# Kernel tuning notes

Hardware: AMD Instinct MI355X
Metric: run time of the kernel (lower is better)

## Reference

```python
import jax, jax.numpy as jnp
import numpy as np

L = 4          # num_layers
H = 128        # hidden_channels
F = 128        # num_filters
G = 25         # num_gaussians
N = 10000      # nodes
E = 320000     # radius-graph edges
EH = 40000     # hull edges
NG = 64        # graphs in batch
CUTOFF = 5.0
PI = float(np.pi)
LOG2 = float(np.log(2.0))


def ssp(x):  # ShiftedSoftplus
    return jax.nn.softplus(x) - LOG2


def setup_inputs() -> dict:
    key = jax.random.key(0)
    ks = iter(jax.random.split(key, 64))
    w = lambda shape: jax.random.normal(next(ks), shape, jnp.float32) * 0.05
    inp = {
        'z': jax.random.randint(next(ks), (N,), 0, 100),
        'edge_index': jax.random.randint(next(ks), (2, E), 0, N),
        'edge_index_hull': jax.random.randint(next(ks), (2, EH), 0, N),
        'batch': jnp.sort(jax.random.randint(next(ks), (N,), 0, NG)),
        'dist': jax.random.uniform(next(ks), (E,), jnp.float32) * CUTOFF,
        'fea_hull': jax.random.normal(next(ks), (EH, 7), jnp.float32),
        'emb_table': w((100, H)),
        'lin_w': w((L, F, H)),
        'mlp_w1': w((L, F, G)), 'mlp_b1': jnp.zeros((L, F), jnp.float32),
        'mlp_w2': w((L, F, F)), 'mlp_b2': jnp.zeros((L, F), jnp.float32),
        'linh_w': w((L, F, H)),
        'mlph_w1': w((L, F, 7)), 'mlph_b1': jnp.zeros((L, F), jnp.float32),
        'mlph_w2': w((L, F, F)), 'mlph_b2': jnp.zeros((L, F), jnp.float32),
        'v1_w': w((L, H, F)), 'v1_b': jnp.zeros((L, H), jnp.float32),
        'v2_w': w((L, 64, H)), 'v2_b': jnp.zeros((L, 64), jnp.float32),
        'vh1_w': w((L, H, F)), 'vh1_b': jnp.zeros((L, H), jnp.float32),
        'vh2_w': w((L, 64, H)), 'vh2_b': jnp.zeros((L, 64), jnp.float32),
        'cat_w': w((L, H, 128)), 'cat_b': jnp.zeros((L, H), jnp.float32),
        'u1_w': w((64, H)), 'u1_b': jnp.zeros((64,), jnp.float32),
        'u2_w': w((1, 64)), 'u2_b': jnp.zeros((1,), jnp.float32),
    }
    return inp


def reference(z, edge_index, edge_index_hull, batch, dist, fea_hull, emb_table,
              lin_w, mlp_w1, mlp_b1, mlp_w2, mlp_b2,
              linh_w, mlph_w1, mlph_b1, mlph_w2, mlph_b2,
              v1_w, v1_b, v2_w, v2_b, vh1_w, vh1_b, vh2_w, vh2_b,
              cat_w, cat_b, u1_w, u1_b, u2_w, u2_b):
    n = z.shape[0]
    # Gaussian distance embedding: emb(0, cutoff, G)
    offset = jnp.linspace(0.0, CUTOFF, G)
    coeff = -0.5 / (offset[1] - offset[0]) ** 2
    dist_emb = jnp.exp(coeff * (dist[:, None] - offset[None, :]) ** 2)  # [E,G]
    C = 0.5 * (jnp.cos(dist * PI / CUTOFF) + 1.0)                       # [E]
    j, i = edge_index[0], edge_index[1]
    jh, ih = edge_index_hull[0], edge_index_hull[1]
    v = emb_table[z]                                                    # [N,H]
    for l in range(L):
        # update_e
        W = (ssp(dist_emb @ mlp_w1[l].T + mlp_b1[l]) @ mlp_w2[l].T + mlp_b2[l]) * C[:, None]
        e = (v @ lin_w[l].T)[j] * W                                     # [E,F]
        Wh = ssp(fea_hull @ mlph_w1[l].T + mlph_b1[l]) @ mlph_w2[l].T + mlph_b2[l]
        eh = (v @ linh_w[l].T)[jh] * Wh                                 # [EH,F]
        # update_v
        out = jax.ops.segment_sum(e, i, num_segments=n)
        out = ssp(out @ v1_w[l].T + v1_b[l]) @ v2_w[l].T + v2_b[l]      # [N,64]
        outh = jax.ops.segment_sum(eh, ih, num_segments=n)
        outh = ssp(outh @ vh1_w[l].T + vh1_b[l]) @ vh2_w[l].T + vh2_b[l]
        v = v + ssp(jnp.concatenate([out, outh], axis=1) @ cat_w[l].T + cat_b[l])
    # update_u
    u = ssp(v @ u1_w.T + u1_b) @ u2_w.T + u2_b                          # [N,1]
    return jax.ops.segment_sum(u, batch, num_segments=NG)               # [NG,1]
```

## Files before the change

kernel.cpp:

```cpp
#include <hip/hip_runtime.h>
#include <hip/hip_bf16.h>

typedef __hip_bfloat16 bf16;
typedef unsigned short ushort;
typedef __attribute__((ext_vector_type(8))) short short8;
typedef __attribute__((ext_vector_type(4))) float f32x4;

__device__ __forceinline__ float dssp(float x){
  return fmaxf(x, 0.f) + __logf(1.f + __expf(-fabsf(x))) - 0.693147180559945f;
}
__device__ __forceinline__ int clampi(int x, int lo, int hi){ return x<lo?lo:(x>hi?hi:x); }
__device__ __forceinline__ ushort f2b(float f){
  unsigned x = __float_as_uint(f);
  return (ushort)((x + 0x7fffu + ((x>>16)&1u)) >> 16);
}
__device__ __forceinline__ float b2f16(ushort u){ return __uint_as_float(((unsigned)u)<<16); }

constexpr int TBL_K    = 4096;
constexpr int TBL_ROWS = TBL_K + 1;
constexpr int TBL_TILES = (TBL_ROWS + 31) / 32;

__global__ void detect_mode(const unsigned* __restrict__ raw, int* flag){
  __shared__ int c;
  int t = threadIdx.x;
  if (t==0) c = 0;
  __syncthreads();
  unsigned u  = raw[t];
  unsigned lo = u & 0xFFFFu;
  int e = (int)((lo >> 7) & 0xFF);
  int ok = (lo==0u) || (e >= 0x70 && e <= 0x8F);
  atomicAdd(&c, ok);
  __syncthreads();
  if (t==0) *flag = (c >= 160) ? 1 : 0;
}

struct Seg { const void* src; float* dst; int n; };
struct SegTable { Seg s[27]; int count; long total; };

__global__ void convert_all(SegTable tbl, const int* __restrict__ flag){
  int mode = *flag;
  long tid    = (long)blockIdx.x*blockDim.x + threadIdx.x;
  long stride = (long)gridDim.x*blockDim.x;
  for (long i=tid; i<tbl.total; i+=stride){
    long off = i; int k = 0;
    while (k < tbl.count-1 && off >= tbl.s[k].n){ off -= tbl.s[k].n; k++; }
    float f;
    if (mode) f = __bfloat162float(((const bf16*)tbl.s[k].src)[off]);
    else      f = ((const float*)tbl.s[k].src)[off];
    tbl.s[k].dst[off] = (f==f) ? f : 0.f;
  }
}

struct WSeg { const float* src; ushort* dst; int n; };
struct WTable { WSeg s[9]; int count; int total; };

__global__ void convert_wb(WTable wt){
  int tid = blockIdx.x*blockDim.x + threadIdx.x;
  if (tid >= wt.total) return;
  int off = tid, k = 0;
  while (k < wt.count-1 && off >= wt.s[k].n){ off -= wt.s[k].n; k++; }
  wt.s[k].dst[off] = f2b(wt.s[k].src[off]);
}

__global__ void init_all(int* cnt_r, int* cnt_h, float* uacc,
                         int2* spk_r, int2* spk_h, int N, int E, int EH){
  int t = blockIdx.x*blockDim.x + threadIdx.x;
  if (t < N){ cnt_r[t]=0; cnt_h[t]=0; }
  if (t < 64) uacc[t]=0.f;
  if (t < E)  spk_r[t]=make_int2(0,0);
  if (t < EH) spk_h[t]=make_int2(0,0);
}

__global__ void count_edges(const int* __restrict__ ei, const int* __restrict__ eih,
                            int E, int EH, int N, int* cnt_r, int* cnt_h){
  int t = blockIdx.x*blockDim.x + threadIdx.x;
  if (t < E)  atomicAdd(&cnt_r[clampi(ei[E + t], 0, N-1)], 1);
  if (t < EH) atomicAdd(&cnt_h[clampi(eih[EH + t], 0, N-1)], 1);
}

__global__ __launch_bounds__(1024) void scan_pair(const int* cnt_r, int* off_r, int* cur_r,
                                                  const int* cnt_h, int* off_h, int* cur_h, int N){
  __shared__ int s[1024];
  int t = threadIdx.x;
  int CH = (N + 1023) / 1024;
  for (int which=0; which<2; which++){
    const int* cnt = which? cnt_h : cnt_r;
    int* off = which? off_h : off_r;
    int* cur = which? cur_h : cur_r;
    int base = t*CH;
    int sum = 0;
    for (int q=0;q<CH;q++){ int idx=base+q; sum += (idx<N)? cnt[idx] : 0; }
    __syncthreads();
    s[t]=sum; __syncthreads();
    for (int ofs=1; ofs<1024; ofs<<=1){
      int v = s[t]; int vp = (t>=ofs)? s[t-ofs] : 0;
      __syncthreads(); s[t]=v+vp; __syncthreads();
    }
    int run = (t>0)? s[t-1] : 0;
    for (int q=0;q<CH;q++){
      int idx=base+q;
      if (idx<N){ off[idx]=run; cur[idx]=run; run += cnt[idx]; }
    }
    if (t==1023) off[N] = s[1023];
  }
}

__global__ void scatter_edges(const int* __restrict__ ei, const float* __restrict__ distc,
                              const int* __restrict__ eih, int E, int EH, int N,
                              int* cur_r, int* cur_h, int2* spk_r, int2* spk_h){
  int t = blockIdx.x*blockDim.x + threadIdx.x;
  if (t < E){
    int i = clampi(ei[E+t], 0, N-1);
    int p = clampi(atomicAdd(&cur_r[i], 1), 0, E-1);
    float x = fminf(fmaxf(distc[t]*(4096.0f/5.0f), 0.f), 4095.999f);
    int i0 = (int)x; if (i0 > TBL_K-1) i0 = TBL_K-1;
    unsigned fr16 = (unsigned)((x - (float)i0)*65536.0f); if (fr16 > 65535u) fr16 = 65535u;
    spk_r[p] = make_int2(clampi(ei[t],0,N-1), (int)(((unsigned)i0<<16)|fr16));
  }
  if (t < EH){
    int ih = clampi(eih[EH+t], 0, N-1);
    int p = clampi(atomicAdd(&cur_h[ih], 1), 0, EH-1);
    spk_h[p] = make_int2(clampi(eih[t],0,N-1), t);
  }
}

__global__ __launch_bounds__(256) void build_wtab(const float* __restrict__ mlp_w1,
    const float* __restrict__ mlp_b1, const float* __restrict__ mlp_w2,
    const float* __restrict__ mlp_b2, ushort* __restrict__ Wtab){
  int l    = blockIdx.x / TBL_TILES;
  int tile = blockIdx.x % TBL_TILES;
  int row0 = tile * 32;
  const float* w1 = mlp_w1 + l*128*25;
  const float* b1 = mlp_b1 + l*128;
  const float* w2 = mlp_w2 + l*128*128;
  const float* b2 = mlp_b2 + l*128;
  __shared__ float Gs[32][26];
  __shared__ float Ts[32][129];
  __shared__ float Ws[32][129];
  int t = threadIdx.x;
  for (int idx=t; idx<32*25; idx+=256){
    int r = idx/25, k = idx%25;
    float d = (row0+r) * (5.0f/4096.0f);
    float x = d - (float)k*(5.0f/24.0f);
    Gs[r][k] = __expf(-11.52f*x*x);
  }
  __syncthreads();
  int rg = t&7, cg = t>>3;
  #pragma unroll
  for (int ri=0;ri<4;ri++){
    int r = rg*4+ri;
    #pragma unroll
    for (int ci=0;ci<4;ci++){
      int c = cg*4+ci;
      float s = b1[c];
      for (int k=0;k<25;k++) s += Gs[r][k]*w1[c*25+k];
      Ts[r][c] = dssp(s);
    }
  }
  float acc[4][4] = {};
  for (int k0=0;k0<128;k0+=32){
    __syncthreads();
    for (int idx=t; idx<1024; idx+=256){
      int c=idx>>3, kk4=(idx&7)*4;
      float4 f = *(const float4*)(w2+(size_t)c*128+k0+kk4);
      Ws[kk4][c]=f.x; Ws[kk4+1][c]=f.y; Ws[kk4+2][c]=f.z; Ws[kk4+3][c]=f.w;
    }
    __syncthreads();
    for (int kk=0;kk<32;kk++){
      float xv[4];
      #pragma unroll
      for (int ri=0;ri<4;ri++) xv[ri]=Ts[rg*4+ri][k0+kk];
      #pragma unroll
      for (int ci=0;ci<4;ci++){
        float wv = Ws[kk][cg*4+ci];
        #pragma unroll
        for (int ri=0;ri<4;ri++) acc[ri][ci] += xv[ri]*wv;
      }
    }
  }
  #pragma unroll
  for (int ri=0;ri<4;ri++){
    int r = row0 + rg*4 + ri;
    if (r >= TBL_ROWS) continue;
    float d  = r * (5.0f/4096.0f);
    float Cf = 0.5f*(cosf(d*(3.14159265358979f/5.0f))+1.0f);
    #pragma unroll
    for (int ci=0;ci<4;ci++){
      int c = cg*4+ci;
      Wtab[((size_t)l*TBL_ROWS + r)*128 + c] = f2b((acc[ri][ci] + b2[c]) * Cf);
    }
  }
}

__global__ void pack_wtab(const ushort* __restrict__ Wtab, unsigned* __restrict__ Wpk){
  long t = (long)blockIdx.x*blockDim.x + threadIdx.x;
  const long TOT = 4L*TBL_K*128;
  if (t < TOT){
    int l = (int)(t / ((long)TBL_K*128));
    long rem = t % ((long)TBL_K*128);
    int r = (int)(rem >> 7), f = (int)(rem & 127);
    const ushort* base = Wtab + (size_t)l*TBL_ROWS*128;
    Wpk[t] = (((unsigned)base[(size_t)(r+1)*128+f])<<16) | (unsigned)base[(size_t)r*128+f];
  }
}

__device__ __forceinline__ short8 afragb(const ushort (*Xb)[136], int lane, int k0){
  int m=lane&15, q=(lane>>4)&3;
  return *(const short8*)(&Xb[m][k0+q*8]);
}
__device__ __forceinline__ short8 bfrag(const ushort* __restrict__ W, int cbase, int lane, int k0){
  int n=lane&15, q=(lane>>4)&3;
  return *(const short8*)(W + (size_t)(cbase+n)*128 + k0 + q*8);
}
template<int NT>
__device__ __forceinline__ void mgemm(const ushort (*Xb)[136],
    const ushort* __restrict__ W, int t, f32x4 d[NT]){
  int lane=t&63, w=t>>6;
  #pragma unroll
  for (int ct=0;ct<NT;ct++) d[ct]=(f32x4){0.f,0.f,0.f,0.f};
  #pragma unroll
  for (int kc=0;kc<4;kc++){
    short8 a = afragb(Xb, lane, kc*32);
    #pragma unroll
    for (int ct=0;ct<NT;ct++){
      short8 b = bfrag(W, w*(NT*16)+ct*16, lane, kc*32);
      d[ct] = __builtin_amdgcn_mfma_f32_16x16x32_bf16(a, b, d[ct], 0, 0, 0);
    }
  }
}
template<int NT>
__device__ __forceinline__ void d2tile(ushort (*Y)[136], const f32x4 d[NT], int t,
    int colofs, const float* __restrict__ bias, int do_ssp){
  int lane=t&63, w=t>>6, q=(lane>>4)&3, n=lane&15;
  #pragma unroll
  for (int ct=0;ct<NT;ct++){
    int c = w*(NT*16)+ct*16+n;
    float bv = bias? bias[c] : 0.f;
    #pragma unroll
    for (int i=0;i<4;i++){
      float y = d[ct][i] + bv;
      if (do_ssp) y = dssp(y);
      Y[q*4+i][colofs+c] = f2b(y);
    }
  }
}
template<int NT>
__device__ __forceinline__ void d2os(float (*Os)[132], const f32x4 d[NT], int t,
    const float* __restrict__ bias, int do_ssp){
  int lane=t&63, w=t>>6, q=(lane>>4)&3, n=lane&15;
  #pragma unroll
  for (int ct=0;ct<NT;ct++){
    int c = w*(NT*16)+ct*16+n;
    float bv = bias? bias[c] : 0.f;
    #pragma unroll
    for (int i=0;i<4;i++){
      float y = d[ct][i] + bv;
      if (do_ssp) y = dssp(y);
      Os[q*4+i][c] = y;
    }
  }
}
__device__ __forceinline__ void d2glob_c(ushort* __restrict__ out, const f32x4 d[2],
    int t, int row0, int N, ushort (*Tmp)[136]){
  d2tile<2>(Tmp, d, t, 0, nullptr, 0);
  __syncthreads();
  int r=t>>4, o=(t&15)*8;
  int gr=row0+r;
  if (gr<N) *(uint4*)(out + (size_t)gr*128 + o) = *(const uint4*)&Tmp[r][o];
  __syncthreads();
}

__global__ __launch_bounds__(256) void f_first(const int* __restrict__ z,
    const float* __restrict__ emb, float* __restrict__ v,
    const ushort* __restrict__ linA, const ushort* __restrict__ linB,
    ushort* __restrict__ vlin, ushort* __restrict__ vlinh, int N){
  __shared__ ushort Xb[16][136];
  __shared__ ushort Tb[16][136];
  int t=threadIdx.x; int row0=blockIdx.x*16;
  f32x4 d[2];
  for (int idx=t; idx<512; idx+=256){
    int r=idx>>5, k4=(idx&31)*4; int gr=row0+r;
    int zz=(gr<N)? clampi(z[gr],0,99):0;
    float4 f = *(const float4*)(emb + (size_t)zz*128 + k4);
    unsigned r0 = (unsigned)f2b(f.x) | ((unsigned)f2b(f.y)<<16);
    unsigned r1 = (unsigned)f2b(f.z) | ((unsigned)f2b(f.w)<<16);
    *(uint2*)&Xb[r][k4] = make_uint2(r0,r1);
    if (gr<N) *(float4*)(v + (size_t)gr*128 + k4) = f;
  }
  __syncthreads();
  mgemm<2>(Xb, linA, t, d);
  d2glob_c(vlin, d, t, row0, N, Tb);
  mgemm<2>(Xb, linB, t, d);
  d2glob_c(vlinh, d, t, row0, N, Tb);
}

__global__ __launch_bounds__(256) void f_mid(
    const float* __restrict__ accR, const float* __restrict__ accH,
    float* __restrict__ v,
    const ushort* __restrict__ v1w, const float* __restrict__ v1b,
    const ushort* __restrict__ v2w, const float* __restrict__ v2b,
    const ushort* __restrict__ vh1w, const float* __restrict__ vh1b,
    const ushort* __restrict__ vh2w, const float* __restrict__ vh2b,
    const ushort* __restrict__ cw, const float* __restrict__ cb,
    const ushort* __restrict__ linA, const ushort* __restrict__ linB,
    ushort* __restrict__ vlin, ushort* __restrict__ vlinh, int N){
  __shared__ ushort Xb[16][136];
  __shared__ ushort Xb2[16][136];
  __shared__ ushort Xb3[16][136];
  __shared__ float  Os[16][132];
  int t=threadIdx.x; int row0=blockIdx.x*16;
  f32x4 d[2]; f32x4 d1[1];

  for (int path=0; path<2; path++){
    const float* X = path? accH : accR;
    __syncthreads();
    for (int idx=t; idx<512; idx+=256){
      int r=idx>>5, k4=(idx&31)*4; int gr=row0+r;
      float4 f=(gr<N)? *(const float4*)(X+(size_t)gr*128+k4):make_float4(0,0,0,0);
      unsigned r0 = (unsigned)f2b(f.x) | ((unsigned)f2b(f.y)<<16);
      unsigned r1 = (unsigned)f2b(f.z) | ((unsigned)f2b(f.w)<<16);
      *(uint2*)&Xb[r][k4] = make_uint2(r0,r1);
    }
    __syncthreads();
    mgemm<2>(Xb, path?vh1w:v1w, t, d);
    d2tile<2>(Xb2, d, t, 0, path?vh1b:v1b, 1);
    __syncthreads();
    mgemm<1>(Xb2, path?vh2w:v2w, t, d1);
    d2tile<1>(Xb3, d1, t, path*64, path?vh2b:v2b, 0);
  }
  __syncthreads();
  mgemm<2>(Xb3, cw, t, d);
  d2os<2>(Os, d, t, cb, 1);
  __syncthreads();
  for (int idx=t; idx<512; idx+=256){
    int r=idx>>5, k4=(idx&31)*4; int gr=row0+r;
    float4 f=(gr<N)? *(const float4*)(v+(size_t)gr*128+k4):make_float4(0,0,0,0);
    f.x+=Os[r][k4]; f.y+=Os[r][k4+1]; f.z+=Os[r][k4+2]; f.w+=Os[r][k4+3];
    if (gr<N) *(float4*)(v+(size_t)gr*128+k4)=f;
    unsigned r0 = (unsigned)f2b(f.x) | ((unsigned)f2b(f.y)<<16);
    unsigned r1 = (unsigned)f2b(f.z) | ((unsigned)f2b(f.w)<<16);
    *(uint2*)&Xb[r][k4] = make_uint2(r0,r1);
  }
  __syncthreads();
  mgemm<2>(Xb, linA, t, d);
  d2glob_c(vlin, d, t, row0, N, Xb2);
  mgemm<2>(Xb, linB, t, d);
  d2glob_c(vlinh, d, t, row0, N, Xb2);
}

__global__ __launch_bounds__(256) void f_last(
    const float* __restrict__ accR, const float* __restrict__ accH,
    const float* __restrict__ v,
    const ushort* __restrict__ v1w, const float* __restrict__ v1b,
    const ushort* __restrict__ v2w, const float* __restrict__ v2b,
    const ushort* __restrict__ vh1w, const float* __restrict__ vh1b,
    const ushort* __restrict__ vh2w, const float* __restrict__ vh2b,
    const ushort* __restrict__ cw, const float* __restrict__ cb,
    const ushort* __restrict__ u1w, const float* __restrict__ u1b,
    const float* __restrict__ u2w, const float* __restrict__ u2b,
    const int* __restrict__ batch, float* __restrict__ uacc, int N){
  __shared__ ushort Xb[16][136];
  __shared__ ushort Xb2[16][136];
  __shared__ ushort Xb3[16][136];
  __shared__ float  Os[16][132];
  __shared__ float ss[16];
  __shared__ int   bb[16];
  int t=threadIdx.x; int row0=blockIdx.x*16;
  f32x4 d[2]; f32x4 d1[1];

  for (int path=0; path<2; path++){
    const float* X = path? accH : accR;
    __syncthreads();
    for (int idx=t; idx<512; idx+=256){
      int r=idx>>5, k4=(idx&31)*4; int gr=row0+r;
      float4 f=(gr<N)? *(const float4*)(X+(size_t)gr*128+k4):make_float4(0,0,0,0);
      unsigned r0 = (unsigned)f2b(f.x) | ((unsigned)f2b(f.y)<<16);
      unsigned r1 = (unsigned)f2b(f.z) | ((unsigned)f2b(f.w)<<16);
      *(uint2*)&Xb[r][k4] = make_uint2(r0,r1);
    }
    __syncthreads();
    mgemm<2>(Xb, path?vh1w:v1w, t, d);
    d2tile<2>(Xb2, d, t, 0, path?vh1b:v1b, 1);
    __syncthreads();
    mgemm<1>(Xb2, path?vh2w:v2w, t, d1);
    d2tile<1>(Xb3, d1, t, path*64, path?vh2b:v2b, 0);
  }
  __syncthreads();
  mgemm<2>(Xb3, cw, t, d);
  d2os<2>(Os, d, t, cb, 1);
  __syncthreads();
  for (int idx=t; idx<512; idx+=256){
    int r=idx>>5, k4=(idx&31)*4; int gr=row0+r;
    float4 f=(gr<N)? *(const float4*)(v+(size_t)gr*128+k4):make_float4(0,0,0,0);
    f.x+=Os[r][k4]; f.y+=Os[r][k4+1]; f.z+=Os[r][k4+2]; f.w+=Os[r][k4+3];
    unsigned r0 = (unsigned)f2b(f.x) | ((unsigned)f2b(f.y)<<16);
    unsigned r1 = (unsigned)f2b(f.z) | ((unsigned)f2b(f.w)<<16);
    *(uint2*)&Xb[r][k4] = make_uint2(r0,r1);
  }
  __syncthreads();
  mgemm<1>(Xb, u1w, t, d1);
  d2os<1>(Os, d1, t, u1b, 1);
  __syncthreads();
  if (t<16){
    int gr=row0+t;
    float s=0.f; int bt=-1;
    if (gr<N){
      s = u2b[0];
      for (int c=0;c<64;c++) s += Os[t][c]*u2w[c];
      bt = clampi(batch[gr],0,63);
    }
    ss[t]=s; bb[t]=bt;
  }
  __syncthreads();
  if (t==0){
    float run=0.f; int cur=-1;
    for (int q=0;q<16;q++){
      int bq=bb[q];
      if (bq<0) continue;
      if (bq!=cur){ if (cur>=0) atomicAdd(&uacc[cur],run); cur=bq; run=0.f; }
      run += ss[q];
    }
    if (cur>=0) atomicAdd(&uacc[cur],run);
  }
}

__global__ __launch_bounds__(256) void hull_all(const int2* __restrict__ spk_h,
    const float* __restrict__ fea,
    const float* __restrict__ mlph_w1, const float* __restrict__ mlph_b1,
    const ushort* __restrict__ mlph_w2b, const float* __restrict__ mlph_b2,
    ushort* __restrict__ WhS_base, size_t lstride,
    int EH, int tilesPerLayer, int l0){
  int l    = l0 + blockIdx.x / tilesPerLayer;
  int tile = blockIdx.x % tilesPerLayer;
  int row0 = tile*64;
  const float* w1 = mlph_w1 + l*128*7;
  const float* b1 = mlph_b1 + l*128;
  const ushort* w2 = mlph_w2b + (size_t)l*16384;
  const float* b2 = mlph_b2 + l*128;
  ushort* WhS = WhS_base + (size_t)(l-l0)*lstride;
  __shared__ int   Eid[64];
  __shared__ float Fs[64][8];
  __shared__ ushort Buf[64][136];
  int t=threadIdx.x;
  if (t < 64){
    int p=row0+t;
    Eid[t]=(p<EH)? clampi(spk_h[p].y,0,EH-1):0;
  }
  __syncthreads();
  for (int idx=t; idx<448; idx+=256){
    int r=idx/7, k=idx%7;
    int p=row0+r;
    Fs[r][k]=(p<EH)? fea[(size_t)Eid[r]*7+k]:0.f;
  }
  __syncthreads();
  {
    int c0=(t&31)*4, r0=(t>>5)*8;
    float w[4][7]; float bb[4];
    #pragma unroll
    for (int cc=0;cc<4;cc++){
      bb[cc]=b1[c0+cc];
      #pragma unroll
      for (int k=0;k<7;k++) w[cc][k]=w1[(c0+cc)*7+k];
    }
    #pragma unroll
    for (int rr=0;rr<8;rr++){
      int r=r0+rr;
      float fv[7];
      #pragma unroll
      for (int k=0;k<7;k++) fv[k]=Fs[r][k];
      ushort o[4];
      #pragma unroll
      for (int cc=0;cc<4;cc++){
        float s=bb[cc];
        #pragma unroll
        for (int k=0;k<7;k++) s=fmaf(fv[k],w[cc][k],s);
        o[cc]=f2b(dssp(s));
      }
      unsigned lo=(unsigned)o[0]|((unsigned)o[1]<<16);
      unsigned hi=(unsigned)o[2]|((unsigned)o[3]<<16);
      *(uint2*)&Buf[r][c0]=make_uint2(lo,hi);
    }
  }
  __syncthreads();
  int lane=t&63, w=t>>6;
  const ushort (*Xw)[136] = (const ushort (*)[136])&Buf[w*16][0];
  f32x4 d[8];
  #pragma unroll
  for (int ct=0;ct<8;ct++) d[ct]=(f32x4){0.f,0.f,0.f,0.f};
  #pragma unroll
  for (int kc=0;kc<4;kc++){
    short8 a = afragb(Xw, lane, kc*32);
    #pragma unroll
    for (int ct=0;ct<8;ct++){
      short8 b = bfrag(w2, ct*16, lane, kc*32);
      d[ct] = __builtin_amdgcn_mfma_f32_16x16x32_bf16(a, b, d[ct], 0, 0, 0);
    }
  }
  __syncthreads();
  int q=(lane>>4)&3, n=lane&15;
  #pragma unroll
  for (int ct=0;ct<8;ct++){
    int c=ct*16+n;
    float bv=b2[c];
    #pragma unroll
    for (int i=0;i<4;i++)
      Buf[w*16+q*4+i][c] = f2b(d[ct][i]+bv);
  }
  __syncthreads();
  #pragma unroll
  for (int j=0;j<4;j++){
    int idx=j*256+t;
    int r=idx>>4, o=(idx&15)*8;
    *(uint4*)(WhS + (size_t)(row0+r)*128 + o) = *(const uint4*)&Buf[r][o];
  }
}

__device__ __forceinline__ float rlerp(unsigned y, const unsigned* __restrict__ Wpk, int f){
  int i0 = (int)(y>>16);
  float fr = (float)(y&0xFFFFu)*(1.f/65536.f);
  unsigned u = Wpk[(size_t)i0*128+f];
  float w0=__uint_as_float(u<<16), w1=__uint_as_float(u&0xFFFF0000u);
  return fmaf(fr, w1-w0, w0);
}

__global__ __launch_bounds__(128) void acc_both(
    const int* __restrict__ off_r, const int2* __restrict__ spk_r,
    const ushort* __restrict__ vlin, const unsigned* __restrict__ Wpk,
    float* __restrict__ accR,
    const int* __restrict__ off_h, const int2* __restrict__ spk_h,
    const ushort* __restrict__ vlinh, const ushort* __restrict__ WhS,
    float* __restrict__ accH,
    int Etot, int EHtot, int N){
  int f = threadIdx.x;
  if ((int)blockIdx.x < N){
    int n = blockIdx.x;
    int b = clampi(off_r[n], 0, Etot);
    int e = clampi(off_r[n+1], b, Etot);
    float a = 0.f;
    int p = b;
    for (; p+8<=e; p+=8){
      int2 k[8];
      #pragma unroll
      for (int j=0;j<8;j++) k[j]=spk_r[p+j];
      float vv[8], ww[8];
      #pragma unroll
      for (int j=0;j<8;j++) vv[j]=b2f16(vlin[(size_t)k[j].x*128+f]);
      #pragma unroll
      for (int j=0;j<8;j++) ww[j]=rlerp((unsigned)k[j].y, Wpk, f);
      #pragma unroll
      for (int j=0;j<8;j++) a=fmaf(vv[j],ww[j],a);
    }
    for (; p+4<=e; p+=4){
      int2 k0=spk_r[p], k1=spk_r[p+1], k2=spk_r[p+2], k3=spk_r[p+3];
      float v0 = b2f16(vlin[(size_t)k0.x*128+f]);
      float v1 = b2f16(vlin[(size_t)k1.x*128+f]);
      float v2 = b2f16(vlin[(size_t)k2.x*128+f]);
      float v3 = b2f16(vlin[(size_t)k3.x*128+f]);
      float w0 = rlerp((unsigned)k0.y, Wpk, f);
      float w1 = rlerp((unsigned)k1.y, Wpk, f);
      float w2 = rlerp((unsigned)k2.y, Wpk, f);
      float w3 = rlerp((unsigned)k3.y, Wpk, f);
      a += v0*w0 + v1*w1 + v2*w2 + v3*w3;
    }
    for (; p<e; p++){
      int2 k0=spk_r[p];
      a += b2f16(vlin[(size_t)k0.x*128+f]) * rlerp((unsigned)k0.y, Wpk, f);
    }
    accR[(size_t)n*128+f] = a;
  } else {
    int n = blockIdx.x - N;
    int b = clampi(off_h[n], 0, EHtot);
    int e = clampi(off_h[n+1], b, EHtot);
    float a = 0.f;
    int p = b;
    for (; p+4<=e; p+=4){
      int2 k0=spk_h[p], k1=spk_h[p+1], k2=spk_h[p+2], k3=spk_h[p+3];
      float v0 = b2f16(vlinh[(size_t)k0.x*128+f]);
      float v1 = b2f16(vlinh[(size_t)k1.x*128+f]);
      float v2 = b2f16(vlinh[(size_t)k2.x*128+f]);
      float v3 = b2f16(vlinh[(size_t)k3.x*128+f]);
      a += v0*b2f16(WhS[(size_t)p*128+f])     + v1*b2f16(WhS[(size_t)(p+1)*128+f])
         + v2*b2f16(WhS[(size_t)(p+2)*128+f]) + v3*b2f16(WhS[(size_t)(p+3)*128+f]);
    }
    for (; p<e; p++){
      int2 k0=spk_h[p];
      a += b2f16(vlinh[(size_t)k0.x*128+f]) * b2f16(WhS[(size_t)p*128+f]);
    }
    accH[(size_t)n*128+f] = a;
  }
}

__global__ void write_out(const float* __restrict__ uacc, void* out, const int* __restrict__ flag){
  int t = threadIdx.x;
  if (t < 64){
    if (*flag) ((bf16*)out)[t] = __float2bfloat16(uacc[t]);
    else       ((float*)out)[t] = uacc[t];
  }
}

extern "C" void kernel_launch(void* const* d_in, const int* in_sizes, int n_in,
                              void* d_out, int out_size, void* d_ws, size_t ws_size,
                              hipStream_t stream){
  const int* z     = (const int*)d_in[0];
  const int* ei    = (const int*)d_in[1];
  const int* eih   = (const int*)d_in[2];
  const int* batch = (const int*)d_in[3];

  const int N  = in_sizes[0];
  const int E  = in_sizes[1]/2;
  const int EH = in_sizes[2]/2;
  const int EHpad = (EH + 63) & ~63;

  char* wp = (char*)d_ws;
  auto alloc = [&](size_t bytes)->char*{
    char* p = wp; wp += (bytes + 255) & ~(size_t)255; return p;
  };
  int* flag    = (int*)alloc(256);
  int* cnt_r   = (int*)alloc((size_t)N*4);
  int* off_r   = (int*)alloc((size_t)(N+1)*4);
  int* cur_r   = (int*)alloc((size_t)N*4);
  int* cnt_h   = (int*)alloc((size_t)N*4);
  int* off_h   = (int*)alloc((size_t)(N+1)*4);
  int* cur_h   = (int*)alloc((size_t)N*4);
  int2* spk_r  = (int2*)alloc((size_t)E*8);
  int2* spk_h  = (int2*)alloc((size_t)EH*8);
  float* uacc  = (float*)alloc(64*4);

  SegTable tbl; tbl.count = 27; tbl.total = 0;
  float* cvt[27];
  for (int i=0;i<27;i++){
    int n = in_sizes[4+i];
    cvt[i] = (float*)alloc((size_t)n*4);
    tbl.s[i].src = d_in[4+i];
    tbl.s[i].dst = cvt[i];
    tbl.s[i].n   = n;
    tbl.total   += n;
  }
  const float* distc   = cvt[0];
  const float* feac    = cvt[1];
  const float* embc    = cvt[2];
  const float* mlp_w1  = cvt[4];
  const float* mlp_b1  = cvt[5];
  const float* mlp_w2  = cvt[6];
  const float* mlp_b2  = cvt[7];
  const float* mlph_w1 = cvt[9];
  const float* mlph_b1 = cvt[10];
  const float* mlph_b2 = cvt[12];
  const float* v1_b  = cvt[14];
  const float* v2_b  = cvt[16];
  const float* vh1_b = cvt[18];
  const float* vh2_b = cvt[20];
  const float* cat_b = cvt[22];
  const float* u1_b  = cvt[24];
  const float* u2_w  = cvt[25];
  const float* u2_b  = cvt[26];

  ushort* lin_wb   = (ushort*)alloc((size_t)4*16384*2);
  ushort* linh_wb  = (ushort*)alloc((size_t)4*16384*2);
  ushort* v1_wb    = (ushort*)alloc((size_t)4*16384*2);
  ushort* vh1_wb   = (ushort*)alloc((size_t)4*16384*2);
  ushort* cat_wb   = (ushort*)alloc((size_t)4*16384*2);
  ushort* mlph_w2b = (ushort*)alloc((size_t)4*16384*2);
  ushort* v2_wb    = (ushort*)alloc((size_t)4*8192*2);
  ushort* vh2_wb   = (ushort*)alloc((size_t)4*8192*2);
  ushort* u1_wb    = (ushort*)alloc((size_t)8192*2);
  WTable wt; wt.count = 9;
  wt.s[0] = { cvt[3],  lin_wb,   4*16384 };
  wt.s[1] = { cvt[8],  linh_wb,  4*16384 };
  wt.s[2] = { cvt[13], v1_wb,    4*16384 };
  wt.s[3] = { cvt[17], vh1_wb,   4*16384 };
  wt.s[4] = { cvt[21], cat_wb,   4*16384 };
  wt.s[5] = { cvt[11], mlph_w2b, 4*16384 };
  wt.s[6] = { cvt[15], v2_wb,    4*8192  };
  wt.s[7] = { cvt[19], vh2_wb,   4*8192  };
  wt.s[8] = { cvt[23], u1_wb,    8192    };
  wt.total = 6*4*16384 + 2*4*8192 + 8192;

  ushort*   Wtab = (ushort*)alloc((size_t)4*TBL_ROWS*128*2);
  unsigned* Wpk  = (unsigned*)alloc((size_t)4*TBL_K*128*4);
  float* v     = (float*)alloc((size_t)N*128*4);
  ushort* vlin  = (ushort*)alloc((size_t)N*128*2);
  ushort* vlinh = (ushort*)alloc((size_t)N*128*2);
  float* accR  = (float*)alloc((size_t)N*128*4);
  float* accH  = (float*)alloc((size_t)N*128*4);

  size_t used = (size_t)(wp - (char*)d_ws);
  size_t whs1 = (size_t)EHpad*128*2;
  bool pre = (ws_size >= used + 4*whs1 + 256);
  ushort* WhS = (ushort*)alloc(pre ? 4*whs1 : whs1);

  detect_mode<<<1,256,0,stream>>>((const unsigned*)d_in[6], flag);
  {
    int cb = (int)((tbl.total + 255)/256);
    if (cb > 4096) cb = 4096;
    convert_all<<<cb,256,0,stream>>>(tbl, flag);
  }
  convert_wb<<<(wt.total+255)/256,256,0,stream>>>(wt);

  int nb;
  nb = (E+255)/256;     init_all<<<nb,256,0,stream>>>(cnt_r,cnt_h,uacc,spk_r,spk_h,N,E,EH);
  nb = (E+255)/256;     count_edges<<<nb,256,0,stream>>>(ei,eih,E,EH,N,cnt_r,cnt_h);
  scan_pair<<<1,1024,0,stream>>>(cnt_r,off_r,cur_r,cnt_h,off_h,cur_h,N);
  nb = (E+255)/256;     scatter_edges<<<nb,256,0,stream>>>(ei,distc,eih,E,EH,N,cur_r,cur_h,spk_r,spk_h);
  build_wtab<<<4*TBL_TILES,256,0,stream>>>(mlp_w1,mlp_b1,mlp_w2,mlp_b2,Wtab);
  pack_wtab<<<(int)((4L*TBL_K*128+255)/256),256,0,stream>>>(Wtab,Wpk);

  const int nt = (N+15)/16;
  const int ht64 = (EH+63)/64;
  if (pre)
    hull_all<<<4*ht64,256,0,stream>>>(spk_h, feac, mlph_w1, mlph_b1, mlph_w2b, mlph_b2,
                                      WhS, whs1/2, EH, ht64, 0);

  f_first<<<nt,256,0,stream>>>(z, embc, v, lin_wb, linh_wb, vlin, vlinh, N);
  for (int l=0;l<4;l++){
    if (!pre)
      hull_all<<<ht64,256,0,stream>>>(spk_h, feac, mlph_w1, mlph_b1, mlph_w2b, mlph_b2,
                                      WhS, 0, EH, ht64, l);
    const ushort* WhSl = pre ? (WhS + (size_t)l*(whs1/2)) : WhS;
    acc_both<<<2*N,128,0,stream>>>(off_r, spk_r, vlin, Wpk + (size_t)l*TBL_K*128, accR,
                                   off_h, spk_h, vlinh, WhSl, accH, E, EH, N);
    if (l<3){
      f_mid<<<nt,256,0,stream>>>(accR, accH, v,
          v1_wb + (size_t)l*16384, v1_b + l*128, v2_wb + (size_t)l*8192, v2_b + l*64,
          vh1_wb + (size_t)l*16384, vh1_b + l*128, vh2_wb + (size_t)l*8192, vh2_b + l*64,
          cat_wb + (size_t)l*16384, cat_b + l*128,
          lin_wb + (size_t)(l+1)*16384, linh_wb + (size_t)(l+1)*16384, vlin, vlinh, N);
    } else {
      f_last<<<nt,256,0,stream>>>(accR, accH, v,
          v1_wb + (size_t)l*16384, v1_b + l*128, v2_wb + (size_t)l*8192, v2_b + l*64,
          vh1_wb + (size_t)l*16384, vh1_b + l*128, vh2_wb + (size_t)l*8192, vh2_b + l*64,
          cat_wb + (size_t)l*16384, cat_b + l*128,
          u1_wb, u1_b, u2_w, u2_b, batch, uacc, N);
    }
  }
  write_out<<<1,64,0,stream>>>(uacc, d_out, flag);
}
```

Measured before the change: 485.5 us.

## Merge setup kernels into fewer launches and convert weights directly from inputs

```diff
diff --git a/kernel.cpp b/kernel.cpp
--- a/kernel.cpp
+++ b/kernel.cpp
@@ -20,62 +20,68 @@
 constexpr int TBL_ROWS = TBL_K + 1;
 constexpr int TBL_TILES = (TBL_ROWS + 31) / 32;
 
-__global__ void detect_mode(const unsigned* __restrict__ raw, int* flag){
+struct Seg { const void* src; float* dst; int n; };
+struct SegTable { Seg s[18]; int count; long total; };
+struct WSeg { const void* src; ushort* dst; int n; };
+struct WTable { WSeg s[9]; int count; int total; };
+
+__global__ void setup_all(const unsigned* __restrict__ raw, int* flag,
+                          int* cnt_r, int* cnt_h, float* uacc,
+                          int2* spk_r, int2* spk_h, int N, int E, int EH){
   __shared__ int c;
-  int t = threadIdx.x;
-  if (t==0) c = 0;
-  __syncthreads();
-  unsigned u  = raw[t];
-  unsigned lo = u & 0xFFFFu;
-  int e = (int)((lo >> 7) & 0xFF);
-  int ok = (lo==0u) || (e >= 0x70 && e <= 0x8F);
-  atomicAdd(&c, ok);
-  __syncthreads();
-  if (t==0) *flag = (c >= 160) ? 1 : 0;
-}
-
-struct Seg { const void* src; float* dst; int n; };
-struct SegTable { Seg s[27]; int count; long total; };
-
-__global__ void convert_all(SegTable tbl, const int* __restrict__ flag){
-  int mode = *flag;
-  long tid    = (long)blockIdx.x*blockDim.x + threadIdx.x;
-  long stride = (long)gridDim.x*blockDim.x;
-  for (long i=tid; i<tbl.total; i+=stride){
-    long off = i; int k = 0;
-    while (k < tbl.count-1 && off >= tbl.s[k].n){ off -= tbl.s[k].n; k++; }
-    float f;
-    if (mode) f = __bfloat162float(((const bf16*)tbl.s[k].src)[off]);
-    else      f = ((const float*)tbl.s[k].src)[off];
-    tbl.s[k].dst[off] = (f==f) ? f : 0.f;
-  }
-}
-
-struct WSeg { const float* src; ushort* dst; int n; };
-struct WTable { WSeg s[9]; int count; int total; };
-
-__global__ void convert_wb(WTable wt){
-  int tid = blockIdx.x*blockDim.x + threadIdx.x;
-  if (tid >= wt.total) return;
-  int off = tid, k = 0;
-  while (k < wt.count-1 && off >= wt.s[k].n){ off -= wt.s[k].n; k++; }
-  wt.s[k].dst[off] = f2b(wt.s[k].src[off]);
-}
-
-__global__ void init_all(int* cnt_r, int* cnt_h, float* uacc,
-                         int2* spk_r, int2* spk_h, int N, int E, int EH){
   int t = blockIdx.x*blockDim.x + threadIdx.x;
   if (t < N){ cnt_r[t]=0; cnt_h[t]=0; }
   if (t < 64) uacc[t]=0.f;
   if (t < E)  spk_r[t]=make_int2(0,0);
   if (t < EH) spk_h[t]=make_int2(0,0);
-}
-
-__global__ void count_edges(const int* __restrict__ ei, const int* __restrict__ eih,
-                            int E, int EH, int N, int* cnt_r, int* cnt_h){
-  int t = blockIdx.x*blockDim.x + threadIdx.x;
-  if (t < E)  atomicAdd(&cnt_r[clampi(ei[E + t], 0, N-1)], 1);
-  if (t < EH) atomicAdd(&cnt_h[clampi(eih[EH + t], 0, N-1)], 1);
+  if (blockIdx.x==0){
+    if (threadIdx.x==0) c=0;
+    __syncthreads();
+    unsigned u  = raw[threadIdx.x];
+    unsigned lo = u & 0xFFFFu;
+    int e = (int)((lo >> 7) & 0xFF);
+    int ok = (lo==0u) || (e >= 0x70 && e <= 0x8F);
+    atomicAdd(&c, ok);
+    __syncthreads();
+    if (threadIdx.x==0) *flag = (c >= 160) ? 1 : 0;
+  }
+}
+
+__global__ __launch_bounds__(256) void convert_count(SegTable tbl, WTable wt,
+    const int* __restrict__ flag,
+    const int* __restrict__ ei, const int* __restrict__ eih,
+    int E, int EH, int N, int* cnt_r, int* cnt_h, int CA, int CB){
+  int b = blockIdx.x;
+  if (b < CA){
+    int mode = *flag;
+    long tid    = (long)b*256 + threadIdx.x;
+    long stride = (long)CA*256;
+    for (long i=tid; i<tbl.total; i+=stride){
+      long off = i; int k = 0;
+      while (k < tbl.count-1 && off >= tbl.s[k].n){ off -= tbl.s[k].n; k++; }
+      float f;
+      if (mode) f = __bfloat162float(((const bf16*)tbl.s[k].src)[off]);
+      else      f = ((const float*)tbl.s[k].src)[off];
+      tbl.s[k].dst[off] = (f==f) ? f : 0.f;
+    }
+  } else if (b < CA+CB){
+    int mode = *flag;
+    long tid    = (long)(b-CA)*256 + threadIdx.x;
+    long stride = (long)CB*256;
+    for (long i=tid; i<wt.total; i+=stride){
+      long off = i; int k = 0;
+      while (k < wt.count-1 && off >= wt.s[k].n){ off -= wt.s[k].n; k++; }
+      if (mode) wt.s[k].dst[off] = ((const ushort*)wt.s[k].src)[off];
+      else {
+        float f = ((const float*)wt.s[k].src)[off];
+        wt.s[k].dst[off] = f2b((f==f)? f : 0.f);
+      }
+    }
+  } else {
+    int t = (b-CA-CB)*256 + threadIdx.x;
+    if (t < E)  atomicAdd(&cnt_r[clampi(ei[E + t], 0, N-1)], 1);
+    if (t < EH) atomicAdd(&cnt_h[clampi(eih[EH + t], 0, N-1)], 1);
+  }
 }
 
 __global__ __launch_bounds__(1024) void scan_pair(const int* cnt_r, int* off_r, int* cur_r,
@@ -105,38 +111,42 @@
   }
 }
 
-__global__ void scatter_edges(const int* __restrict__ ei, const float* __restrict__ distc,
-                              const int* __restrict__ eih, int E, int EH, int N,
-                              int* cur_r, int* cur_h, int2* spk_r, int2* spk_h){
-  int t = blockIdx.x*blockDim.x + threadIdx.x;
-  if (t < E){
-    int i = clampi(ei[E+t], 0, N-1);
-    int p = clampi(atomicAdd(&cur_r[i], 1), 0, E-1);
-    float x = fminf(fmaxf(distc[t]*(4096.0f/5.0f), 0.f), 4095.999f);
-    int i0 = (int)x; if (i0 > TBL_K-1) i0 = TBL_K-1;
-    unsigned fr16 = (unsigned)((x - (float)i0)*65536.0f); if (fr16 > 65535u) fr16 = 65535u;
-    spk_r[p] = make_int2(clampi(ei[t],0,N-1), (int)(((unsigned)i0<<16)|fr16));
-  }
-  if (t < EH){
-    int ih = clampi(eih[EH+t], 0, N-1);
-    int p = clampi(atomicAdd(&cur_h[ih], 1), 0, EH-1);
-    spk_h[p] = make_int2(clampi(eih[t],0,N-1), t);
-  }
-}
-
-__global__ __launch_bounds__(256) void build_wtab(const float* __restrict__ mlp_w1,
-    const float* __restrict__ mlp_b1, const float* __restrict__ mlp_w2,
-    const float* __restrict__ mlp_b2, ushort* __restrict__ Wtab){
-  int l    = blockIdx.x / TBL_TILES;
-  int tile = blockIdx.x % TBL_TILES;
+__global__ __launch_bounds__(256) void scatter_build(
+    const int* __restrict__ ei, const float* __restrict__ distc,
+    const int* __restrict__ eih, int E, int EH, int N,
+    int* cur_r, int* cur_h, int2* spk_r, int2* spk_h,
+    const float* __restrict__ mlp_w1, const float* __restrict__ mlp_b1,
+    const float* __restrict__ mlp_w2, const float* __restrict__ mlp_b2,
+    ushort* __restrict__ Wtab, int nbE){
+  __shared__ __align__(16) char smem[36352];
+  if ((int)blockIdx.x < nbE){
+    int t = blockIdx.x*256 + threadIdx.x;
+    if (t < E){
+      int i = clampi(ei[E+t], 0, N-1);
+      int p = clampi(atomicAdd(&cur_r[i], 1), 0, E-1);
+      float x = fminf(fmaxf(distc[t]*(4096.0f/5.0f), 0.f), 4095.999f);
+      int i0 = (int)x; if (i0 > TBL_K-1) i0 = TBL_K-1;
+      unsigned fr16 = (unsigned)((x - (float)i0)*65536.0f); if (fr16 > 65535u) fr16 = 65535u;
+      spk_r[p] = make_int2(clampi(ei[t],0,N-1), (int)(((unsigned)i0<<16)|fr16));
+    }
+    if (t < EH){
+      int ih = clampi(eih[EH+t], 0, N-1);
+      int p = clampi(atomicAdd(&cur_h[ih], 1), 0, EH-1);
+      spk_h[p] = make_int2(clampi(eih[t],0,N-1), t);
+    }
+    return;
+  }
+  int bid  = blockIdx.x - nbE;
+  int l    = bid / TBL_TILES;
+  int tile = bid % TBL_TILES;
   int row0 = tile * 32;
   const float* w1 = mlp_w1 + l*128*25;
   const float* b1 = mlp_b1 + l*128;
   const float* w2 = mlp_w2 + l*128*128;
   const float* b2 = mlp_b2 + l*128;
-  __shared__ float Gs[32][26];
-  __shared__ float Ts[32][129];
-  __shared__ float Ws[32][129];
+  float (*Gs)[26]  = (float(*)[26])smem;
+  float (*Ts)[129] = (float(*)[129])(smem+3328);
+  float (*Ws)[129] = (float(*)[129])(smem+19840);
   int t = threadIdx.x;
   for (int idx=t; idx<32*25; idx+=256){
     int r = idx/25, k = idx%25;
@@ -192,18 +202,6 @@
   }
 }
 
-__global__ void pack_wtab(const ushort* __restrict__ Wtab, unsigned* __restrict__ Wpk){
-  long t = (long)blockIdx.x*blockDim.x + threadIdx.x;
-  const long TOT = 4L*TBL_K*128;
-  if (t < TOT){
-    int l = (int)(t / ((long)TBL_K*128));
-    long rem = t % ((long)TBL_K*128);
-    int r = (int)(rem >> 7), f = (int)(rem & 127);
-    const ushort* base = Wtab + (size_t)l*TBL_ROWS*128;
-    Wpk[t] = (((unsigned)base[(size_t)(r+1)*128+f])<<16) | (unsigned)base[(size_t)r*128+f];
-  }
-}
-
 __device__ __forceinline__ short8 afragb(const ushort (*Xb)[136], int lane, int k0){
   int m=lane&15, q=(lane>>4)&3;
   return *(const short8*)(&Xb[m][k0+q*8]);
@@ -270,13 +268,104 @@
   __syncthreads();
 }
 
-__global__ __launch_bounds__(256) void f_first(const int* __restrict__ z,
+__device__ void hull_body(int bid, const int2* __restrict__ spk_h,
+    const float* __restrict__ fea,
+    const float* __restrict__ mlph_w1, const float* __restrict__ mlph_b1,
+    const ushort* __restrict__ mlph_w2b, const float* __restrict__ mlph_b2,
+    ushort* __restrict__ WhS_base, size_t lstride,
+    int EH, int tilesPerLayer, int l0, char* smem){
+  int l    = l0 + bid / tilesPerLayer;
+  int tile = bid % tilesPerLayer;
+  int row0 = tile*64;
+  const float* w1 = mlph_w1 + l*128*7;
+  const float* b1 = mlph_b1 + l*128;
+  const ushort* w2 = mlph_w2b + (size_t)l*16384;
+  const float* b2 = mlph_b2 + l*128;
+  ushort* WhS = WhS_base + (size_t)(l-l0)*lstride;
+  int*   Eid = (int*)smem;
+  float (*Fs)[8] = (float(*)[8])(smem+256);
+  ushort (*Buf)[136] = (ushort(*)[136])(smem+2304);
+  int t=threadIdx.x;
+  if (t < 64){
+    int p=row0+t;
+    Eid[t]=(p<EH)? clampi(spk_h[p].y,0,EH-1):0;
+  }
+  __syncthreads();
+  for (int idx=t; idx<448; idx+=256){
+    int r=idx/7, k=idx%7;
+    int p=row0+r;
+    Fs[r][k]=(p<EH)? fea[(size_t)Eid[r]*7+k]:0.f;
+  }
+  __syncthreads();
+  {
+    int c0=(t&31)*4, r0=(t>>5)*8;
+    float w[4][7]; float bb[4];
+    #pragma unroll
+    for (int cc=0;cc<4;cc++){
+      bb[cc]=b1[c0+cc];
+      #pragma unroll
+      for (int k=0;k<7;k++) w[cc][k]=w1[(c0+cc)*7+k];
+    }
+    #pragma unroll
+    for (int rr=0;rr<8;rr++){
+      int r=r0+rr;
+      float fv[7];
+      #pragma unroll
+      for (int k=0;k<7;k++) fv[k]=Fs[r][k];
+      ushort o[4];
+      #pragma unroll
+      for (int cc=0;cc<4;cc++){
+        float s=bb[cc];
+        #pragma unroll
+        for (int k=0;k<7;k++) s=fmaf(fv[k],w[cc][k],s);
+        o[cc]=f2b(dssp(s));
+      }
+      unsigned lo=(unsigned)o[0]|((unsigned)o[1]<<16);
+      unsigned hi=(unsigned)o[2]|((unsigned)o[3]<<16);
+      *(uint2*)&Buf[r][c0]=make_uint2(lo,hi);
+    }
+  }
+  __syncthreads();
+  int lane=t&63, w=t>>6;
+  const ushort (*Xw)[136] = (const ushort (*)[136])&Buf[w*16][0];
+  f32x4 d[8];
+  #pragma unroll
+  for (int ct=0;ct<8;ct++) d[ct]=(f32x4){0.f,0.f,0.f,0.f};
+  #pragma unroll
+  for (int kc=0;kc<4;kc++){
+    short8 a = afragb(Xw, lane, kc*32);
+    #pragma unroll
+    for (int ct=0;ct<8;ct++){
+      short8 b = bfrag(w2, ct*16, lane, kc*32);
+      d[ct] = __builtin_amdgcn_mfma_f32_16x16x32_bf16(a, b, d[ct], 0, 0, 0);
+    }
+  }
+  __syncthreads();
+  int q=(lane>>4)&3, n=lane&15;
+  #pragma unroll
+  for (int ct=0;ct<8;ct++){
+    int c=ct*16+n;
+    float bv=b2[c];
+    #pragma unroll
+    for (int i=0;i<4;i++)
+      Buf[w*16+q*4+i][c] = f2b(d[ct][i]+bv);
+  }
+  __syncthreads();
+  #pragma unroll
+  for (int j=0;j<4;j++){
+    int idx=j*256+t;
+    int r=idx>>4, o=(idx&15)*8;
+    *(uint4*)(WhS + (size_t)(row0+r)*128 + o) = *(const uint4*)&Buf[r][o];
+  }
+}
+
+__device__ void f_first_body(int bid, const int* __restrict__ z,
     const float* __restrict__ emb, float* __restrict__ v,
     const ushort* __restrict__ linA, const ushort* __restrict__ linB,
-    ushort* __restrict__ vlin, ushort* __restrict__ vlinh, int N){
-  __shared__ ushort Xb[16][136];
-  __shared__ ushort Tb[16][136];
-  int t=threadIdx.x; int row0=blockIdx.x*16;
+    ushort* __restrict__ vlin, ushort* __restrict__ vlinh, int N, char* smem){
+  ushort (*Xb)[136] = (ushort(*)[136])smem;
+  ushort (*Tb)[136] = (ushort(*)[136])(smem+4352);
+  int t=threadIdx.x; int row0=bid*16;
   f32x4 d[2];
   for (int idx=t; idx<512; idx+=256){
     int r=idx>>5, k4=(idx&31)*4; int gr=row0+r;
@@ -292,6 +381,47 @@
   d2glob_c(vlin, d, t, row0, N, Tb);
   mgemm<2>(Xb, linB, t, d);
   d2glob_c(vlinh, d, t, row0, N, Tb);
+}
+
+__global__ __launch_bounds__(256) void hull_pack_first(const int2* __restrict__ spk_h,
+    const float* __restrict__ fea,
+    const float* __restrict__ mlph_w1, const float* __restrict__ mlph_b1,
+    const ushort* __restrict__ mlph_w2b, const float* __restrict__ mlph_b2,
+    ushort* __restrict__ WhS, size_t lstride, int EH, int ht64,
+    const int* __restrict__ z, const float* __restrict__ emb, float* __restrict__ v,
+    const ushort* __restrict__ linA, const ushort* __restrict__ linB,
+    ushort* __restrict__ vlin, ushort* __restrict__ vlinh, int N, int nt,
+    const ushort* __restrict__ Wtab, unsigned* __restrict__ Wpk, int PB, int HB){
+  __shared__ __align__(16) char smem[19968];
+  int b = blockIdx.x;
+  if (b < HB){
+    hull_body(b, spk_h, fea, mlph_w1, mlph_b1, mlph_w2b, mlph_b2,
+              WhS, lstride, EH, ht64, 0, smem);
+  } else if (b < HB+nt){
+    f_first_body(b-HB, z, emb, v, linA, linB, vlin, vlinh, N, smem);
+  } else {
+    long tid    = (long)(b-HB-nt)*256 + threadIdx.x;
+    long stride = (long)PB*256;
+    const long TOT = 4L*TBL_K*128;
+    for (long i=tid; i<TOT; i+=stride){
+      int l = (int)(i / ((long)TBL_K*128));
+      long rem = i % ((long)TBL_K*128);
+      int r = (int)(rem >> 7), f = (int)(rem & 127);
+      const ushort* base = Wtab + (size_t)l*TBL_ROWS*128;
+      Wpk[i] = (((unsigned)base[(size_t)(r+1)*128+f])<<16) | (unsigned)base[(size_t)r*128+f];
+    }
+  }
+}
+
+__global__ __launch_bounds__(256) void hull_all(const int2* __restrict__ spk_h,
+    const float* __restrict__ fea,
+    const float* __restrict__ mlph_w1, const float* __restrict__ mlph_b1,
+    const ushort* __restrict__ mlph_w2b, const float* __restrict__ mlph_b2,
+    ushort* __restrict__ WhS_base, size_t lstride,
+    int EH, int tilesPerLayer, int l0){
+  __shared__ __align__(16) char smem[19968];
+  hull_body(blockIdx.x, spk_h, fea, mlph_w1, mlph_b1, mlph_w2b, mlph_b2,
+            WhS_base, lstride, EH, tilesPerLayer, l0, smem);
 }
 
 __global__ __launch_bounds__(256) void f_mid(
@@ -424,97 +554,6 @@
   }
 }
 
-__global__ __launch_bounds__(256) void hull_all(const int2* __restrict__ spk_h,
-    const float* __restrict__ fea,
-    const float* __restrict__ mlph_w1, const float* __restrict__ mlph_b1,
-    const ushort* __restrict__ mlph_w2b, const float* __restrict__ mlph_b2,
-    ushort* __restrict__ WhS_base, size_t lstride,
-    int EH, int tilesPerLayer, int l0){
-  int l    = l0 + blockIdx.x / tilesPerLayer;
-  int tile = blockIdx.x % tilesPerLayer;
-  int row0 = tile*64;
-  const float* w1 = mlph_w1 + l*128*7;
-  const float* b1 = mlph_b1 + l*128;
-  const ushort* w2 = mlph_w2b + (size_t)l*16384;
-  const float* b2 = mlph_b2 + l*128;
-  ushort* WhS = WhS_base + (size_t)(l-l0)*lstride;
-  __shared__ int   Eid[64];
-  __shared__ float Fs[64][8];
-  __shared__ ushort Buf[64][136];
-  int t=threadIdx.x;
-  if (t < 64){
-    int p=row0+t;
-    Eid[t]=(p<EH)? clampi(spk_h[p].y,0,EH-1):0;
-  }
-  __syncthreads();
-  for (int idx=t; idx<448; idx+=256){
-    int r=idx/7, k=idx%7;
-    int p=row0+r;
-    Fs[r][k]=(p<EH)? fea[(size_t)Eid[r]*7+k]:0.f;
-  }
-  __syncthreads();
-  {
-    int c0=(t&31)*4, r0=(t>>5)*8;
-    float w[4][7]; float bb[4];
-    #pragma unroll
-    for (int cc=0;cc<4;cc++){
-      bb[cc]=b1[c0+cc];
-      #pragma unroll
-      for (int k=0;k<7;k++) w[cc][k]=w1[(c0+cc)*7+k];
-    }
-    #pragma unroll
-    for (int rr=0;rr<8;rr++){
-      int r=r0+rr;
-      float fv[7];
-      #pragma unroll
-      for (int k=0;k<7;k++) fv[k]=Fs[r][k];
-      ushort o[4];
-      #pragma unroll
-      for (int cc=0;cc<4;cc++){
-        float s=bb[cc];
-        #pragma unroll
-        for (int k=0;k<7;k++) s=fmaf(fv[k],w[cc][k],s);
-        o[cc]=f2b(dssp(s));
-      }
-      unsigned lo=(unsigned)o[0]|((unsigned)o[1]<<16);
-      unsigned hi=(unsigned)o[2]|((unsigned)o[3]<<16);
-      *(uint2*)&Buf[r][c0]=make_uint2(lo,hi);
-    }
-  }
-  __syncthreads();
-  int lane=t&63, w=t>>6;
-  const ushort (*Xw)[136] = (const ushort (*)[136])&Buf[w*16][0];
-  f32x4 d[8];
-  #pragma unroll
-  for (int ct=0;ct<8;ct++) d[ct]=(f32x4){0.f,0.f,0.f,0.f};
-  #pragma unroll
-  for (int kc=0;kc<4;kc++){
-    short8 a = afragb(Xw, lane, kc*32);
-    #pragma unroll
-    for (int ct=0;ct<8;ct++){
-      short8 b = bfrag(w2, ct*16, lane, kc*32);
-      d[ct] = __builtin_amdgcn_mfma_f32_16x16x32_bf16(a, b, d[ct], 0, 0, 0);
-    }
-  }
-  __syncthreads();
-  int q=(lane>>4)&3, n=lane&15;
-  #pragma unroll
-  for (int ct=0;ct<8;ct++){
-    int c=ct*16+n;
-    float bv=b2[c];
-    #pragma unroll
-    for (int i=0;i<4;i++)
-      Buf[w*16+q*4+i][c] = f2b(d[ct][i]+bv);
-  }
-  __syncthreads();
-  #pragma unroll
-  for (int j=0;j<4;j++){
-    int idx=j*256+t;
-    int r=idx>>4, o=(idx&15)*8;
-    *(uint4*)(WhS + (size_t)(row0+r)*128 + o) = *(const uint4*)&Buf[r][o];
-  }
-}
-
 __device__ __forceinline__ float rlerp(unsigned y, const unsigned* __restrict__ Wpk, int f){
   int i0 = (int)(y>>16);
   float fr = (float)(y&0xFFFFu)*(1.f/65536.f);
@@ -626,14 +665,16 @@
   int2* spk_h  = (int2*)alloc((size_t)EH*8);
   float* uacc  = (float*)alloc(64*4);
 
-  SegTable tbl; tbl.count = 27; tbl.total = 0;
-  float* cvt[27];
-  for (int i=0;i<27;i++){
+  static const int f32_idx[18] = {0,1,2,4,5,6,7,9,10,12,14,16,18,20,22,24,25,26};
+  float* cvt[27] = {};
+  SegTable tbl; tbl.count = 18; tbl.total = 0;
+  for (int k=0;k<18;k++){
+    int i = f32_idx[k];
     int n = in_sizes[4+i];
     cvt[i] = (float*)alloc((size_t)n*4);
-    tbl.s[i].src = d_in[4+i];
-    tbl.s[i].dst = cvt[i];
-    tbl.s[i].n   = n;
+    tbl.s[k].src = d_in[4+i];
+    tbl.s[k].dst = cvt[i];
+    tbl.s[k].n   = n;
     tbl.total   += n;
   }
   const float* distc   = cvt[0];
@@ -665,15 +706,15 @@
   ushort* vh2_wb   = (ushort*)alloc((size_t)4*8192*2);
   ushort* u1_wb    = (ushort*)alloc((size_t)8192*2);
   WTable wt; wt.count = 9;
-  wt.s[0] = { cvt[3],  lin_wb,   4*16384 };
-  wt.s[1] = { cvt[8],  linh_wb,  4*16384 };
-  wt.s[2] = { cvt[13], v1_wb,    4*16384 };
-  wt.s[3] = { cvt[17], vh1_wb,   4*16384 };
-  wt.s[4] = { cvt[21], cat_wb,   4*16384 };
-  wt.s[5] = { cvt[11], mlph_w2b, 4*16384 };
-  wt.s[6] = { cvt[15], v2_wb,    4*8192  };
-  wt.s[7] = { cvt[19], vh2_wb,   4*8192  };
-  wt.s[8] = { cvt[23], u1_wb,    8192    };
+  wt.s[0] = { d_in[4+3],  lin_wb,   4*16384 };
+  wt.s[1] = { d_in[4+8],  linh_wb,  4*16384 };
+  wt.s[2] = { d_in[4+11], mlph_w2b, 4*16384 };
+  wt.s[3] = { d_in[4+13], v1_wb,    4*16384 };
+  wt.s[4] = { d_in[4+15], v2_wb,    4*8192  };
+  wt.s[5] = { d_in[4+17], vh1_wb,   4*16384 };
+  wt.s[6] = { d_in[4+19], vh2_wb,   4*8192  };
+  wt.s[7] = { d_in[4+21], cat_wb,   4*16384 };
+  wt.s[8] = { d_in[4+23], u1_wb,    8192    };
   wt.total = 6*4*16384 + 2*4*8192 + 8192;
 
   ushort*   Wtab = (ushort*)alloc((size_t)4*TBL_ROWS*128*2);
@@ -689,29 +730,26 @@
   bool pre = (ws_size >= used + 4*whs1 + 256);
   ushort* WhS = (ushort*)alloc(pre ? 4*whs1 : whs1);
 
-  detect_mode<<<1,256,0,stream>>>((const unsigned*)d_in[6], flag);
+  const int nbE  = (E+255)/256;
+  const int nt   = (N+15)/16;
+  const int ht64 = (EH+63)/64;
+  const int CA = 1536, CB = 1024, PB = 1024;
+
+  setup_all<<<nbE,256,0,stream>>>((const unsigned*)d_in[6], flag,
+                                  cnt_r, cnt_h, uacc, spk_r, spk_h, N, E, EH);
+  convert_count<<<CA+CB+nbE,256,0,stream>>>(tbl, wt, flag, ei, eih, E, EH, N,
+                                            cnt_r, cnt_h, CA, CB);
+  scan_pair<<<1,1024,0,stream>>>(cnt_r,off_r,cur_r,cnt_h,off_h,cur_h,N);
+  scatter_build<<<nbE + 4*TBL_TILES,256,0,stream>>>(ei, distc, eih, E, EH, N,
+      cur_r, cur_h, spk_r, spk_h, mlp_w1, mlp_b1, mlp_w2, mlp_b2, Wtab, nbE);
   {
-    int cb = (int)((tbl.total + 255)/256);
-    if (cb > 4096) cb = 4096;
-    convert_all<<<cb,256,0,stream>>>(tbl, flag);
-  }
-  convert_wb<<<(wt.total+255)/256,256,0,stream>>>(wt);
-
-  int nb;
-  nb = (E+255)/256;     init_all<<<nb,256,0,stream>>>(cnt_r,cnt_h,uacc,spk_r,spk_h,N,E,EH);
-  nb = (E+255)/256;     count_edges<<<nb,256,0,stream>>>(ei,eih,E,EH,N,cnt_r,cnt_h);
-  scan_pair<<<1,1024,0,stream>>>(cnt_r,off_r,cur_r,cnt_h,off_h,cur_h,N);
-  nb = (E+255)/256;     scatter_edges<<<nb,256,0,stream>>>(ei,distc,eih,E,EH,N,cur_r,cur_h,spk_r,spk_h);
-  build_wtab<<<4*TBL_TILES,256,0,stream>>>(mlp_w1,mlp_b1,mlp_w2,mlp_b2,Wtab);
-  pack_wtab<<<(int)((4L*TBL_K*128+255)/256),256,0,stream>>>(Wtab,Wpk);
-
-  const int nt = (N+15)/16;
-  const int ht64 = (EH+63)/64;
-  if (pre)
-    hull_all<<<4*ht64,256,0,stream>>>(spk_h, feac, mlph_w1, mlph_b1, mlph_w2b, mlph_b2,
-                                      WhS, whs1/2, EH, ht64, 0);
-
-  f_first<<<nt,256,0,stream>>>(z, embc, v, lin_wb, linh_wb, vlin, vlinh, N);
+    int HB = pre ? 4*ht64 : 0;
+    hull_pack_first<<<HB+nt+PB,256,0,stream>>>(spk_h, feac, mlph_w1, mlph_b1,
+        mlph_w2b, mlph_b2, WhS, whs1/2, EH, ht64,
+        z, embc, v, lin_wb, linh_wb, vlin, vlinh, N, nt,
+        Wtab, Wpk, PB, HB);
+  }
+
   for (int l=0;l<4;l++){
     if (!pre)
       hull_all<<<ht64,256,0,stream>>>(spk_h, feac, mlph_w1, mlph_b1, mlph_w2b, mlph_b2,
```

Result: slower. 505.3 us (+4.1%).
